# Performance work log

Measured on AMD Instinct MI355X. Metric: run time of the kernel, lower is better.

Reference implementation:

```python
import jax, jax.numpy as jnp
import numpy as np
from jax import lax

T, I, H = 8192, 1024, 1024


def setup_inputs() -> dict:
    key = jax.random.key(0)
    ks = jax.random.split(key, 7)
    s = 1.0 / np.sqrt(H)
    x = jax.random.normal(ks[0], (T, I), dtype=jnp.float32)
    W_ih = jax.random.uniform(ks[1], (4 * H, I), minval=-s, maxval=s, dtype=jnp.float32)
    W_hh = jax.random.uniform(ks[2], (4 * H, H), minval=-s, maxval=s, dtype=jnp.float32)
    b_ih = jax.random.uniform(ks[3], (4 * H,), minval=-s, maxval=s, dtype=jnp.float32)
    b_hh = jax.random.uniform(ks[4], (4 * H,), minval=-s, maxval=s, dtype=jnp.float32)
    h0 = jax.random.normal(ks[5], (H,), dtype=jnp.float32)
    c0 = jax.random.uniform(ks[6], (H,), dtype=jnp.float32)
    return {"x": x, "W_ih": W_ih, "W_hh": W_hh, "b_ih": b_ih, "b_hh": b_hh, "h0": h0, "c0": c0}


def reference(x, W_ih, W_hh, b_ih, b_hh, h0, c0):
    # Precompute the input contribution to all gates in one big GEMM: [T, 4H]
    gates_x = x @ W_ih.T + (b_ih + b_hh)

    def step(carry, gx):
        h, c = carry
        g = gx + h @ W_hh.T  # [4H]
        i, f, gc, o = jnp.split(g, 4)  # PyTorch gate order: input, forget, cell, output
        i = jax.nn.sigmoid(i)
        f = jax.nn.sigmoid(f)
        gc = jnp.tanh(gc)
        o = jax.nn.sigmoid(o)
        c_new = f * c + i * gc
        h_new = o * jnp.tanh(c_new)
        return (h_new, c_new), h_new

    (_, _), hs = lax.scan(step, (h0, c0), gates_x)
    return hs  # [T, H] — the per-timestep outputs collected in fullDataOutput
```

## Files before the change

kernel.cpp:

```cpp
#include <hip/hip_runtime.h>
#include <cstdint>

#define T_STEPS 8192
#define HDIM    1024
#define NBLK    256
#define NTHR    256

typedef float        f32x4 __attribute__((ext_vector_type(4)));
typedef unsigned int u32x4 __attribute__((ext_vector_type(4)));

__device__ __forceinline__ float dot4(f32x4 a, f32x4 b) {
    return a[0] * b[0] + a[1] * b[1] + a[2] * b[2] + a[3] * b[3];
}
__device__ __forceinline__ float sigmoidf_(float v) { return 1.0f / (1.0f + __expf(-v)); }
__device__ __forceinline__ float tanhf_(float v)    { return 1.0f - 2.0f / (__expf(2.0f * v) + 1.0f); }
__device__ __forceinline__ unsigned bf16_rne(float f) {
    unsigned b = __float_as_uint(f);
    return (b + 0x7FFFu + ((b >> 16) & 1u)) >> 16;
}

#define BAR() do {                                            \
    asm volatile("s_waitcnt lgkmcnt(0)" ::: "memory");        \
    __builtin_amdgcn_sched_barrier(0);                        \
    __builtin_amdgcn_s_barrier();                             \
    __builtin_amdgcn_sched_barrier(0);                        \
} while (0)

__global__ __launch_bounds__(NTHR, 1)
void lstm_persistent(const float* __restrict__ x,
                     const float* __restrict__ W_ih,
                     const float* __restrict__ W_hh,
                     const float* __restrict__ b_ih,
                     const float* __restrict__ b_hh,
                     const float* __restrict__ h0,
                     const float* __restrict__ c0,
                     float* __restrict__ out,
                     unsigned int* __restrict__ ring)
{
    __shared__ float h_lds[2][HDIM];

    const int tid = threadIdx.x;
    const int w   = tid >> 6;
    const int l   = tid & 63;
    const int u   = (blockIdx.x << 2) + w;

    f32x4 whh[16], wih[16];
#pragma unroll
    for (int q = 0; q < 4; ++q) {
        const float* rh = W_hh + (size_t)(q * HDIM + u) * HDIM + 4 * l;
        const float* ri = W_ih + (size_t)(q * HDIM + u) * HDIM + 4 * l;
#pragma unroll
        for (int i = 0; i < 4; ++i) {
            whh[q * 4 + i] = *(const f32x4*)(rh + 256 * i);
            wih[q * 4 + i] = *(const f32x4*)(ri + 256 * i);
        }
    }
#pragma unroll
    for (int k = 0; k < 16; ++k) {
        asm volatile("" : "+v"(whh[k]));
        asm volatile("" : "+v"(wih[k]));
    }

    float bias[4];
#pragma unroll
    for (int q = 0; q < 4; ++q) bias[q] = b_ih[q * HDIM + u] + b_hh[q * HDIM + u];
    float c = c0[u];

    f32x4 hr[4];
#pragma unroll
    for (int i = 0; i < 4; ++i) hr[i] = *(const f32x4*)(h0 + 4 * l + 256 * i);

    float gxp[4];
    {
        f32x4 x0[4];
#pragma unroll
        for (int i = 0; i < 4; ++i) x0[i] = *(const f32x4*)(x + 4 * l + 256 * i);
#pragma unroll
        for (int q = 0; q < 4; ++q) {
            float a = 0.f;
#pragma unroll
            for (int i = 0; i < 4; ++i) a += dot4(wih[q * 4 + i], x0[i]);
            gxp[q] = a;
        }
    }
    f32x4 xr[4], xn[4];
#pragma unroll
    for (int i = 0; i < 4; ++i) xr[i] = *(const f32x4*)(x + HDIM + 4 * l + 256 * i);

    for (int t = 0; t < T_STEPS; ++t) {
        float acc[4];
#pragma unroll
        for (int q = 0; q < 4; ++q) {
            float a = gxp[q];
#pragma unroll
            for (int i = 0; i < 4; ++i) a += dot4(whh[q * 4 + i], hr[i]);
            acc[q] = a;
        }
#pragma unroll
        for (int m = 1; m < 64; m <<= 1) {
#pragma unroll
            for (int q = 0; q < 4; ++q) acc[q] += __shfl_xor(acc[q], m, 64);
        }
        const float gi = sigmoidf_(acc[0] + bias[0]);
        const float gf = sigmoidf_(acc[1] + bias[1]);
        const float gg = tanhf_   (acc[2] + bias[2]);
        const float go = sigmoidf_(acc[3] + bias[3]);
        c = gf * c + gi * gg;
        const float hval = go * tanhf_(c);

        if (l == 0) {
            const unsigned pk = ((unsigned)(t + 1) << 16) | bf16_rne(hval);
            unsigned int* slot = ring + (((t & 1) * NBLK + blockIdx.x) << 4) + w;
            asm volatile("global_store_dword %0, %1, off sc0 sc1"
                         :: "v"((unsigned long long)slot), "v"(pk) : "memory");
            out[(size_t)t * HDIM + u] = hval;
        }
        if (t == T_STEPS - 1) break;

        const unsigned e = (unsigned)(t + 1);
        const unsigned long long base =
            (unsigned long long)(ring + (((t & 1) * NBLK + tid) << 4));

        u32x4 p;
        asm volatile("global_load_dwordx4 %0, %1, off sc0 sc1"
                     : "=v"(p) : "v"(base));

#pragma unroll
        for (int q = 0; q < 4; ++q) {
            float a = 0.f;
#pragma unroll
            for (int i = 0; i < 4; ++i) a += dot4(wih[q * 4 + i], xr[i]);
            gxp[q] = a;
        }

        asm volatile("s_waitcnt vmcnt(0)" : "+v"(p) :: "memory");
        __builtin_amdgcn_sched_barrier(0);
        while (!((p[0] >> 16) == e && (p[1] >> 16) == e &&
                 (p[2] >> 16) == e && (p[3] >> 16) == e)) {
            asm volatile(
                "global_load_dwordx4 %0, %1, off sc0 sc1\n\t"
                "s_waitcnt vmcnt(0)"
                : "=&v"(p) : "v"(base) : "memory");
        }

        {
            const int tn = (t + 2 < T_STEPS) ? (t + 2) : (T_STEPS - 1);
            const float* xp = x + (size_t)tn * HDIM;
#pragma unroll
            for (int i = 0; i < 4; ++i) xn[i] = *(const f32x4*)(xp + 4 * l + 256 * i);
        }
        {
            const int ns = (t + 1) & 1;
            f32x4 hv;
            hv[0] = __uint_as_float(p[0] << 16);
            hv[1] = __uint_as_float(p[1] << 16);
            hv[2] = __uint_as_float(p[2] << 16);
            hv[3] = __uint_as_float(p[3] << 16);
            *(f32x4*)&h_lds[ns][4 * tid] = hv;
        }
        BAR();
        {
            const int ns = (t + 1) & 1;
#pragma unroll
            for (int i = 0; i < 4; ++i)
                hr[i] = *(const f32x4*)&h_lds[ns][4 * l + 256 * i];
        }
#pragma unroll
        for (int i = 0; i < 4; ++i) xr[i] = xn[i];
    }
}

extern "C" void kernel_launch(void* const* d_in, const int* in_sizes, int n_in,
                              void* d_out, int out_size, void* d_ws, size_t ws_size,
                              hipStream_t stream)
{
    const float* x    = (const float*)d_in[0];
    const float* W_ih = (const float*)d_in[1];
    const float* W_hh = (const float*)d_in[2];
    const float* b_ih = (const float*)d_in[3];
    const float* b_hh = (const float*)d_in[4];
    const float* h0   = (const float*)d_in[5];
    const float* c0   = (const float*)d_in[6];

    unsigned int* ring = (unsigned int*)d_ws;
    hipMemsetAsync(d_ws, 0, 2 * NBLK * 16 * sizeof(unsigned int), stream);
    lstm_persistent<<<NBLK, NTHR, 0, stream>>>(x, W_ih, W_hh, b_ih, b_hh, h0, c0,
                                               (float*)d_out, ring);
}
```

Before: 26.44 ms.

## Stage outputs per block contiguously, unroll steps by two, transpose in second kernel

Per-step hval outputs are written to a per-block staging buffer, where each block's four units for a timestep are contiguous and timesteps follow one another, instead of scattered writes into the [T,H] output. A second kernel then transposes the staged data into the final layout. The step loop is unrolled by two with ping-pong x registers, which removes the register copy. The ring poll is restructured so the load issues after the input-gate precompute, and the output store is moved after the wait. The aim is to take uncoalesced output stores off the recurrent critical path, at the cost of an extra kernel launch and an extra pass over the output.

```diff
diff --git a/kernel.cpp b/kernel.cpp
--- a/kernel.cpp
+++ b/kernel.cpp
@@ -25,6 +25,78 @@
     __builtin_amdgcn_s_barrier();                             \
     __builtin_amdgcn_sched_barrier(0);                        \
 } while (0)
+
+#define STEP_BODY(T_, XR_, XN_)                                               \
+{                                                                             \
+    const int t_ = (T_);                                                      \
+    float acc[4];                                                             \
+    _Pragma("unroll")                                                         \
+    for (int q = 0; q < 4; ++q) {                                             \
+        float a = gxp[q];                                                     \
+        _Pragma("unroll")                                                     \
+        for (int i = 0; i < 4; ++i) a += dot4(whh[q * 4 + i], hr[i]);         \
+        acc[q] = a;                                                           \
+    }                                                                         \
+    _Pragma("unroll")                                                         \
+    for (int m = 1; m < 64; m <<= 1) {                                        \
+        _Pragma("unroll")                                                     \
+        for (int q = 0; q < 4; ++q) acc[q] += __shfl_xor(acc[q], m, 64);      \
+    }                                                                         \
+    const float gi = sigmoidf_(acc[0] + bias[0]);                             \
+    const float gf = sigmoidf_(acc[1] + bias[1]);                             \
+    const float gg = tanhf_   (acc[2] + bias[2]);                             \
+    const float go = sigmoidf_(acc[3] + bias[3]);                             \
+    c = gf * c + gi * gg;                                                     \
+    const float hval = go * tanhf_(c);                                        \
+    if (l == 0) {                                                             \
+        const unsigned pk = ((unsigned)(t_ + 1) << 16) | bf16_rne(hval);      \
+        unsigned int* slot = ring + (((t_ & 1) * NBLK + blockIdx.x) << 4) + w;\
+        asm volatile("global_store_dword %0, %1, off sc0 sc1"                 \
+                     :: "v"((unsigned long long)slot), "v"(pk) : "memory");   \
+    }                                                                         \
+    _Pragma("unroll")                                                         \
+    for (int q = 0; q < 4; ++q) {                                             \
+        float a = 0.f;                                                        \
+        _Pragma("unroll")                                                     \
+        for (int i = 0; i < 4; ++i) a += dot4(wih[q * 4 + i], XR_[i]);        \
+        gxp[q] = a;                                                           \
+    }                                                                         \
+    {                                                                         \
+        const unsigned e = (unsigned)(t_ + 1);                                \
+        const unsigned long long base =                                       \
+            (unsigned long long)(ring + (((t_ & 1) * NBLK + tid) << 4));      \
+        u32x4 p;                                                              \
+        for (;;) {                                                            \
+            asm volatile("global_load_dwordx4 %0, %1, off sc0 sc1\n\t"        \
+                         "s_waitcnt vmcnt(0)"                                 \
+                         : "=&v"(p) : "v"(base) : "memory");                  \
+            if ((p[0] >> 16) == e && (p[1] >> 16) == e &&                     \
+                (p[2] >> 16) == e && (p[3] >> 16) == e) break;                \
+        }                                                                     \
+        const int ns = (t_ + 1) & 1;                                          \
+        f32x4 hv;                                                             \
+        hv[0] = __uint_as_float(p[0] << 16);                                  \
+        hv[1] = __uint_as_float(p[1] << 16);                                  \
+        hv[2] = __uint_as_float(p[2] << 16);                                  \
+        hv[3] = __uint_as_float(p[3] << 16);                                  \
+        *(f32x4*)&h_lds[ns][4 * tid] = hv;                                    \
+    }                                                                         \
+    if (l == 0) stagb[t_ * 4 + w] = hval;                                     \
+    {                                                                         \
+        const int tn = (t_ + 2 < T_STEPS) ? (t_ + 2) : (T_STEPS - 1);         \
+        const float* xp = x + (size_t)tn * HDIM;                              \
+        _Pragma("unroll")                                                     \
+        for (int i = 0; i < 4; ++i)                                           \
+            XN_[i] = *(const f32x4*)(xp + 4 * l + 256 * i);                   \
+    }                                                                         \
+    BAR();                                                                    \
+    {                                                                         \
+        const int ns = (t_ + 1) & 1;                                          \
+        _Pragma("unroll")                                                     \
+        for (int i = 0; i < 4; ++i)                                           \
+            hr[i] = *(const f32x4*)&h_lds[ns][4 * l + 256 * i];               \
+    }                                                                         \
+}
 
 __global__ __launch_bounds__(NTHR, 1)
 void lstm_persistent(const float* __restrict__ x,
@@ -34,7 +106,7 @@
                      const float* __restrict__ b_hh,
                      const float* __restrict__ h0,
                      const float* __restrict__ c0,
-                     float* __restrict__ out,
+                     float* __restrict__ stag,
                      unsigned int* __restrict__ ring)
 {
     __shared__ float h_lds[2][HDIM];
@@ -83,91 +155,48 @@
             gxp[q] = a;
         }
     }
-    f32x4 xr[4], xn[4];
-#pragma unroll
-    for (int i = 0; i < 4; ++i) xr[i] = *(const f32x4*)(x + HDIM + 4 * l + 256 * i);
-
-    for (int t = 0; t < T_STEPS; ++t) {
-        float acc[4];
-#pragma unroll
-        for (int q = 0; q < 4; ++q) {
-            float a = gxp[q];
-#pragma unroll
-            for (int i = 0; i < 4; ++i) a += dot4(whh[q * 4 + i], hr[i]);
-            acc[q] = a;
+    f32x4 xA[4], xB[4];
+#pragma unroll
+    for (int i = 0; i < 4; ++i) xA[i] = *(const f32x4*)(x + HDIM + 4 * l + 256 * i);
+
+    float* stagb = stag + (size_t)blockIdx.x * T_STEPS * 4;
+
+    for (int t2 = 0; t2 < T_STEPS; t2 += 2) {
+        STEP_BODY(t2, xA, xB);
+        if (t2 + 1 == T_STEPS - 1) {
+            float acc[4];
+#pragma unroll
+            for (int q = 0; q < 4; ++q) {
+                float a = gxp[q];
+#pragma unroll
+                for (int i = 0; i < 4; ++i) a += dot4(whh[q * 4 + i], hr[i]);
+                acc[q] = a;
+            }
+#pragma unroll
+            for (int m = 1; m < 64; m <<= 1) {
+#pragma unroll
+                for (int q = 0; q < 4; ++q) acc[q] += __shfl_xor(acc[q], m, 64);
+            }
+            const float gi = sigmoidf_(acc[0] + bias[0]);
+            const float gf = sigmoidf_(acc[1] + bias[1]);
+            const float gg = tanhf_   (acc[2] + bias[2]);
+            const float go = sigmoidf_(acc[3] + bias[3]);
+            c = gf * c + gi * gg;
+            const float hval = go * tanhf_(c);
+            if (l == 0) stagb[(T_STEPS - 1) * 4 + w] = hval;
+            break;
         }
-#pragma unroll
-        for (int m = 1; m < 64; m <<= 1) {
-#pragma unroll
-            for (int q = 0; q < 4; ++q) acc[q] += __shfl_xor(acc[q], m, 64);
-        }
-        const float gi = sigmoidf_(acc[0] + bias[0]);
-        const float gf = sigmoidf_(acc[1] + bias[1]);
-        const float gg = tanhf_   (acc[2] + bias[2]);
-        const float go = sigmoidf_(acc[3] + bias[3]);
-        c = gf * c + gi * gg;
-        const float hval = go * tanhf_(c);
-
-        if (l == 0) {
-            const unsigned pk = ((unsigned)(t + 1) << 16) | bf16_rne(hval);
-            unsigned int* slot = ring + (((t & 1) * NBLK + blockIdx.x) << 4) + w;
-            asm volatile("global_store_dword %0, %1, off sc0 sc1"
-                         :: "v"((unsigned long long)slot), "v"(pk) : "memory");
-            out[(size_t)t * HDIM + u] = hval;
-        }
-        if (t == T_STEPS - 1) break;
-
-        const unsigned e = (unsigned)(t + 1);
-        const unsigned long long base =
-            (unsigned long long)(ring + (((t & 1) * NBLK + tid) << 4));
-
-        u32x4 p;
-        asm volatile("global_load_dwordx4 %0, %1, off sc0 sc1"
-                     : "=v"(p) : "v"(base));
-
-#pragma unroll
-        for (int q = 0; q < 4; ++q) {
-            float a = 0.f;
-#pragma unroll
-            for (int i = 0; i < 4; ++i) a += dot4(wih[q * 4 + i], xr[i]);
-            gxp[q] = a;
-        }
-
-        asm volatile("s_waitcnt vmcnt(0)" : "+v"(p) :: "memory");
-        __builtin_amdgcn_sched_barrier(0);
-        while (!((p[0] >> 16) == e && (p[1] >> 16) == e &&
-                 (p[2] >> 16) == e && (p[3] >> 16) == e)) {
-            asm volatile(
-                "global_load_dwordx4 %0, %1, off sc0 sc1\n\t"
-                "s_waitcnt vmcnt(0)"
-                : "=&v"(p) : "v"(base) : "memory");
-        }
-
-        {
-            const int tn = (t + 2 < T_STEPS) ? (t + 2) : (T_STEPS - 1);
-            const float* xp = x + (size_t)tn * HDIM;
-#pragma unroll
-            for (int i = 0; i < 4; ++i) xn[i] = *(const f32x4*)(xp + 4 * l + 256 * i);
-        }
-        {
-            const int ns = (t + 1) & 1;
-            f32x4 hv;
-            hv[0] = __uint_as_float(p[0] << 16);
-            hv[1] = __uint_as_float(p[1] << 16);
-            hv[2] = __uint_as_float(p[2] << 16);
-            hv[3] = __uint_as_float(p[3] << 16);
-            *(f32x4*)&h_lds[ns][4 * tid] = hv;
-        }
-        BAR();
-        {
-            const int ns = (t + 1) & 1;
-#pragma unroll
-            for (int i = 0; i < 4; ++i)
-                hr[i] = *(const f32x4*)&h_lds[ns][4 * l + 256 * i];
-        }
-#pragma unroll
-        for (int i = 0; i < 4; ++i) xr[i] = xn[i];
-    }
+        STEP_BODY(t2 + 1, xB, xA);
+    }
+}
+
+__global__ __launch_bounds__(256)
+void untranspose(const float* __restrict__ stag, float* __restrict__ out)
+{
+    const int t = blockIdx.x;
+    const int b = threadIdx.x;
+    f32x4 v = *(const f32x4*)(stag + (size_t)b * T_STEPS * 4 + t * 4);
+    *(f32x4*)(out + (size_t)t * HDIM + 4 * b) = v;
 }
 
 extern "C" void kernel_launch(void* const* d_in, const int* in_sizes, int n_in,
@@ -183,7 +212,10 @@
     const float* c0   = (const float*)d_in[6];
 
     unsigned int* ring = (unsigned int*)d_ws;
+    float* stag = (float*)((char*)d_ws + (1u << 20));
+
     hipMemsetAsync(d_ws, 0, 2 * NBLK * 16 * sizeof(unsigned int), stream);
     lstm_persistent<<<NBLK, NTHR, 0, stream>>>(x, W_ih, W_hh, b_ih, b_hh, h0, c0,
-                                               (float*)d_out, ring);
-}
+                                               stag, ring);
+    untranspose<<<T_STEPS, 256, 0, stream>>>(stag, (float*)d_out);
+}
```

New measurement: 35.67 ms. +34.9%, slower.
